# Kernel optimization log

Hardware: AMD Instinct MI355X
Metric: run time of the kernel (lower is better)

## Reference

```python
import jax, jax.numpy as jnp
import numpy as np

HIDDEN = 128
INPUT_DIM = 1
NUM_CLASSES = 2


def setup_inputs() -> dict:
    key = jax.random.key(0)
    ks = jax.random.split(key, 7)
    B, T = 256, 1024
    s_ih = 1.0 / np.sqrt(HIDDEN)
    x = jax.random.normal(ks[0], (B, T, INPUT_DIM), dtype=jnp.float32)
    W_ih = jax.random.uniform(ks[1], (HIDDEN, INPUT_DIM), jnp.float32, -s_ih, s_ih)
    W_hh = jax.random.uniform(ks[2], (HIDDEN, HIDDEN), jnp.float32, -s_ih, s_ih)
    b_ih = jax.random.uniform(ks[3], (HIDDEN,), jnp.float32, -s_ih, s_ih)
    b_hh = jax.random.uniform(ks[4], (HIDDEN,), jnp.float32, -s_ih, s_ih)
    W_fc = jax.random.uniform(ks[5], (NUM_CLASSES, HIDDEN), jnp.float32, -s_ih, s_ih)
    b_fc = jax.random.uniform(ks[6], (NUM_CLASSES,), jnp.float32, -s_ih, s_ih)
    return {"x": x, "W_ih": W_ih, "W_hh": W_hh, "b_ih": b_ih,
            "b_hh": b_hh, "W_fc": W_fc, "b_fc": b_fc}


def reference(x, W_ih, W_hh, b_ih, b_hh, W_fc, b_fc):
    B = x.shape[0]
    # Precompute input projection for all timesteps: [B,T,H]
    xp = jnp.einsum('bti,hi->bth', x, W_ih) + b_ih + b_hh
    h0 = jnp.zeros((B, HIDDEN), dtype=x.dtype)

    def step(h, xp_t):
        h_new = jnp.tanh(xp_t + h @ W_hh.T)  # [B,H]
        return h_new, h_new

    _, hs = jax.lax.scan(step, h0, jnp.swapaxes(xp, 0, 1))  # hs: [T,B,H]
    out = jnp.swapaxes(hs, 0, 1)  # [B,T,H]
    logits = jnp.einsum('bth,ch->btc', out, W_fc) + b_fc  # [B,T,C]
    return logits
```

## Files before the change

kernel.cpp:

```cpp
#include <hip/hip_runtime.h>

typedef float f32x2 __attribute__((ext_vector_type(2)));
typedef float f32x4 __attribute__((ext_vector_type(4)));

#define BB 256
#define TT 1024
#define HH 128
#define CC 2

__device__ __forceinline__ float ftanh(float u) {
    float e = __expf(2.0f * u);
    float r = __builtin_amdgcn_rcpf(e + 1.0f);
    return fmaf(-2.0f, r, 1.0f);
}

__device__ __forceinline__ float bcast(float v, int j) {
    return __int_as_float(__builtin_amdgcn_readlane(__float_as_int(v), j));
}

#define DPP_ADD(v, ctrl)                                                     \
    ((v) + __int_as_float(__builtin_amdgcn_mov_dpp(                          \
         __float_as_int(v), (ctrl), 0xF, 0xF, true)))

__global__ __launch_bounds__(256, 1) void rnn_kernel(
    const float* __restrict__ x, const float* __restrict__ W_ih,
    const float* __restrict__ W_hh, const float* __restrict__ b_ih,
    const float* __restrict__ b_hh, const float* __restrict__ W_fc,
    const float* __restrict__ b_fc, float* __restrict__ out)
{
    const int b   = blockIdx.x;
    const int tid = threadIdx.x;
    const int l   = tid & 63;
    const int wv  = tid >> 6;
    const int lq  = l & 31;
    const int kb  = wv << 5;
    const int rA  = l, rB = l + 64;
    const int rF  = kb + lq;

    __shared__ float xs[TT + 8];
    __shared__ f32x2 p2[2][4][64];
    __shared__ f32x2 qp[4][4];
    __shared__ f32x2 obuf[16];

    {
        const f32x4* xr = (const f32x4*)(x + (size_t)b * TT);
        ((f32x4*)xs)[tid] = xr[tid];
    }
    if (tid < 8) xs[TT + tid] = 0.f;

    const float wih  = W_ih[rF];
    const float bias = b_ih[rF] + b_hh[rF];
    const float wfs  = (l < 32) ? W_fc[rF] : W_fc[HH + rF];
    const float bf0  = b_fc[0], bf1 = b_fc[1];

    float wa[32], wb[32];
    {
        const f32x4* a4 = (const f32x4*)(W_hh + (size_t)rA * HH + kb);
        const f32x4* b4 = (const f32x4*)(W_hh + (size_t)rB * HH + kb);
        #pragma unroll
        for (int j = 0; j < 8; ++j) {
            f32x4 va = a4[j], vb = b4[j];
            wa[4*j+0] = va.x; wa[4*j+1] = va.y; wa[4*j+2] = va.z; wa[4*j+3] = va.w;
            wb[4*j+0] = vb.x; wb[4*j+1] = vb.y; wb[4*j+2] = vb.z; wb[4*j+3] = vb.w;
        }
        #pragma unroll
        for (int k = 0; k < 32; ++k)
            asm volatile("" : "+v"(wa[k]), "+v"(wb[k]));
    }

    float hn = 0.f;
    float* o = out + (size_t)b * TT * CC;

    __syncthreads();
    float xcur = xs[0];

    #pragma unroll 4
    for (int t = 0; t < TT; ++t) {
        const int buf = t & 1, qb = t & 3;

        float aA0 = 0.f, aA1 = 0.f, aB0 = 0.f, aB1 = 0.f;
        #pragma unroll
        for (int k = 0; k < 32; k += 2) {
            float s0 = bcast(hn, k);
            float s1 = bcast(hn, k + 1);
            aA0 = fmaf(wa[k],     s0, aA0);
            aB0 = fmaf(wb[k],     s0, aB0);
            aA1 = fmaf(wa[k + 1], s1, aA1);
            aB1 = fmaf(wb[k + 1], s1, aB1);
        }
        p2[buf][wv][l] = f32x2{ aA0 + aA1, aB0 + aB1 };
        const float xnext = xs[t + 1];

        __syncthreads();

        const float* pf = (const float*)&p2[buf][0][0]
                        + ((((wv & 1) << 5) + lq) << 1) + (wv >> 1);
        float p0 = pf[0], p1 = pf[128], pv2 = pf[256], pv3 = pf[384];

        {
            float q = wfs * hn;
            q = DPP_ADD(q, 0xB1);
            q = DPP_ADD(q, 0x4E);
            q = DPP_ADD(q, 0x124);
            q = DPP_ADD(q, 0x128);
            float q0 = bcast(q, 0)  + bcast(q, 16);
            float q1 = bcast(q, 32) + bcast(q, 48);
            if (l == 0) qp[qb][wv] = f32x2{q0, q1};
        }
        if (t >= 2 && tid == 0) {
            const int pq = (t - 1) & 3;
            f32x2 s = (qp[pq][0] + qp[pq][1]) + (qp[pq][2] + qp[pq][3]);
            s.x += bf0; s.y += bf1;
            obuf[(t - 2) & 15] = s;
        }
        if ((t & 15) == 1 && t >= 17 && tid < 32) {
            ((float*)(o + (t - 17) * CC))[tid] = ((const float*)obuf)[tid];
        }

        const float base = fmaf(xcur, wih, bias);
        xcur = xnext;
        hn = ftanh(base + ((p0 + p1) + (pv2 + pv3)));
    }

    {
        float q = wfs * hn;
        q = DPP_ADD(q, 0xB1);
        q = DPP_ADD(q, 0x4E);
        q = DPP_ADD(q, 0x124);
        q = DPP_ADD(q, 0x128);
        float q0 = bcast(q, 0)  + bcast(q, 16);
        float q1 = bcast(q, 32) + bcast(q, 48);
        if (l == 0) qp[0][wv] = f32x2{q0, q1};
    }
    __syncthreads();
    if (tid == 0) {
        f32x2 s = (qp[3][0] + qp[3][1]) + (qp[3][2] + qp[3][3]);
        s.x += bf0; s.y += bf1;
        *(f32x2*)(o + (TT - 2) * CC) = s;
        f32x2 s2 = (qp[0][0] + qp[0][1]) + (qp[0][2] + qp[0][3]);
        s2.x += bf0; s2.y += bf1;
        *(f32x2*)(o + (TT - 1) * CC) = s2;
    }
    if (tid < 28) {
        ((float*)(o + 1008 * CC))[tid] = ((const float*)obuf)[tid];
    }
}

extern "C" void kernel_launch(void* const* d_in, const int* in_sizes, int n_in,
                              void* d_out, int out_size, void* d_ws, size_t ws_size,
                              hipStream_t stream) {
    const float* x    = (const float*)d_in[0];
    const float* W_ih = (const float*)d_in[1];
    const float* W_hh = (const float*)d_in[2];
    const float* b_ih = (const float*)d_in[3];
    const float* b_hh = (const float*)d_in[4];
    const float* W_fc = (const float*)d_in[5];
    const float* b_fc = (const float*)d_in[6];
    float* out = (float*)d_out;

    rnn_kernel<<<BB, 256, 0, stream>>>(x, W_ih, W_hh, b_ih, b_hh, W_fc, b_fc, out);
}
```

Measured before the change: 441.7 us.

## Run each batch row's recurrence in one wavefront with LDS hidden-state ring

Each batch row now uses a single 64-lane wavefront that holds the full W_hh (two rows per lane, 256 VGPRs) instead of four wavefronts that split the K dimension. The new hidden state goes into a 16-deep LDS ring and is read back as float4 broadcasts, with packed f32x2 FMAs. This removes the per-step __syncthreads and the cross-wave partial-sum exchange. The output projection is batched every 16 steps across lanes. The risks are heavy register pressure, with possible spills, and LDS read latency on the serial critical path. Correctness also relies on a single wave giving implicit ordering of LDS accesses without barriers.

```diff
diff --git a/kernel.cpp b/kernel.cpp
--- a/kernel.cpp
+++ b/kernel.cpp
@@ -14,135 +14,100 @@
     return fmaf(-2.0f, r, 1.0f);
 }
 
-__device__ __forceinline__ float bcast(float v, int j) {
-    return __int_as_float(__builtin_amdgcn_readlane(__float_as_int(v), j));
+__device__ __forceinline__ f32x2 pkfma(f32x2 a, f32x2 b, f32x2 c) {
+    return (f32x2){fmaf(a.x, b.x, c.x), fmaf(a.y, b.y, c.y)};
 }
 
-#define DPP_ADD(v, ctrl)                                                     \
-    ((v) + __int_as_float(__builtin_amdgcn_mov_dpp(                          \
-         __float_as_int(v), (ctrl), 0xF, 0xF, true)))
-
-__global__ __launch_bounds__(256, 1) void rnn_kernel(
+__global__ __launch_bounds__(64, 1) void rnn_kernel(
     const float* __restrict__ x, const float* __restrict__ W_ih,
     const float* __restrict__ W_hh, const float* __restrict__ b_ih,
     const float* __restrict__ b_hh, const float* __restrict__ W_fc,
     const float* __restrict__ b_fc, float* __restrict__ out)
 {
-    const int b   = blockIdx.x;
-    const int tid = threadIdx.x;
-    const int l   = tid & 63;
-    const int wv  = tid >> 6;
-    const int lq  = l & 31;
-    const int kb  = wv << 5;
-    const int rA  = l, rB = l + 64;
-    const int rF  = kb + lq;
+    const int b = blockIdx.x;
+    const int l = threadIdx.x;
 
-    __shared__ float xs[TT + 8];
-    __shared__ f32x2 p2[2][4][64];
-    __shared__ f32x2 qp[4][4];
-    __shared__ f32x2 obuf[16];
+    __shared__ float xs[TT + 4];
+    __shared__ float hring[16][132];
 
     {
         const f32x4* xr = (const f32x4*)(x + (size_t)b * TT);
-        ((f32x4*)xs)[tid] = xr[tid];
+        f32x4* xd = (f32x4*)xs;
+        #pragma unroll
+        for (int i = 0; i < 4; ++i) xd[i * 64 + l] = xr[i * 64 + l];
     }
-    if (tid < 8) xs[TT + tid] = 0.f;
+    if (l < 4) xs[TT + l] = 0.f;
+    hring[15][l] = 0.f;
+    hring[15][l + 64] = 0.f;
 
-    const float wih  = W_ih[rF];
-    const float bias = b_ih[rF] + b_hh[rF];
-    const float wfs  = (l < 32) ? W_fc[rF] : W_fc[HH + rF];
-    const float bf0  = b_fc[0], bf1 = b_fc[1];
-
-    float wa[32], wb[32];
+    f32x2 wA[64], wB[64];
     {
-        const f32x4* a4 = (const f32x4*)(W_hh + (size_t)rA * HH + kb);
-        const f32x4* b4 = (const f32x4*)(W_hh + (size_t)rB * HH + kb);
+        const f32x2* a2 = (const f32x2*)(W_hh + (size_t)l * HH);
+        const f32x2* b2 = (const f32x2*)(W_hh + (size_t)(l + 64) * HH);
         #pragma unroll
-        for (int j = 0; j < 8; ++j) {
-            f32x4 va = a4[j], vb = b4[j];
-            wa[4*j+0] = va.x; wa[4*j+1] = va.y; wa[4*j+2] = va.z; wa[4*j+3] = va.w;
-            wb[4*j+0] = vb.x; wb[4*j+1] = vb.y; wb[4*j+2] = vb.z; wb[4*j+3] = vb.w;
-        }
+        for (int j = 0; j < 64; ++j) { wA[j] = a2[j]; wB[j] = b2[j]; }
         #pragma unroll
-        for (int k = 0; k < 32; ++k)
-            asm volatile("" : "+v"(wa[k]), "+v"(wb[k]));
+        for (int j = 0; j < 64; ++j)
+            asm volatile("" : "+v"(wA[j]), "+v"(wB[j]));
     }
 
-    float hn = 0.f;
+    const f32x2 wih2  = (f32x2){W_ih[l], W_ih[l + 64]};
+    const f32x2 bias2 = (f32x2){b_ih[l] + b_hh[l], b_ih[l + 64] + b_hh[l + 64]};
+
+    const int lc = l & 1;
+    const int lt = (l >> 1) & 15;
+    const int lh = l >> 5;
+    const f32x4* wf4 = (const f32x4*)(W_fc + lc * HH + lh * 64);
+    const float bfc = b_fc[lc];
     float* o = out + (size_t)b * TT * CC;
 
     __syncthreads();
+
     float xcur = xs[0];
 
-    #pragma unroll 4
     for (int t = 0; t < TT; ++t) {
-        const int buf = t & 1, qb = t & 3;
+        const f32x4* h4 = (const f32x4*)hring[(t + 15) & 15];
 
-        float aA0 = 0.f, aA1 = 0.f, aB0 = 0.f, aB1 = 0.f;
+        f32x2 aA0 = (f32x2){0.f, 0.f}, aA1 = aA0, aB0 = aA0, aB1 = aA0;
         #pragma unroll
-        for (int k = 0; k < 32; k += 2) {
-            float s0 = bcast(hn, k);
-            float s1 = bcast(hn, k + 1);
-            aA0 = fmaf(wa[k],     s0, aA0);
-            aB0 = fmaf(wb[k],     s0, aB0);
-            aA1 = fmaf(wa[k + 1], s1, aA1);
-            aB1 = fmaf(wb[k + 1], s1, aB1);
-        }
-        p2[buf][wv][l] = f32x2{ aA0 + aA1, aB0 + aB1 };
-        const float xnext = xs[t + 1];
-
-        __syncthreads();
-
-        const float* pf = (const float*)&p2[buf][0][0]
-                        + ((((wv & 1) << 5) + lq) << 1) + (wv >> 1);
-        float p0 = pf[0], p1 = pf[128], pv2 = pf[256], pv3 = pf[384];
-
-        {
-            float q = wfs * hn;
-            q = DPP_ADD(q, 0xB1);
-            q = DPP_ADD(q, 0x4E);
-            q = DPP_ADD(q, 0x124);
-            q = DPP_ADD(q, 0x128);
-            float q0 = bcast(q, 0)  + bcast(q, 16);
-            float q1 = bcast(q, 32) + bcast(q, 48);
-            if (l == 0) qp[qb][wv] = f32x2{q0, q1};
-        }
-        if (t >= 2 && tid == 0) {
-            const int pq = (t - 1) & 3;
-            f32x2 s = (qp[pq][0] + qp[pq][1]) + (qp[pq][2] + qp[pq][3]);
-            s.x += bf0; s.y += bf1;
-            obuf[(t - 2) & 15] = s;
-        }
-        if ((t & 15) == 1 && t >= 17 && tid < 32) {
-            ((float*)(o + (t - 17) * CC))[tid] = ((const float*)obuf)[tid];
+        for (int j = 0; j < 32; ++j) {
+            const f32x4 hv = h4[j];
+            const f32x2 hlo = (f32x2){hv.x, hv.y};
+            const f32x2 hhi = (f32x2){hv.z, hv.w};
+            aA0 = pkfma(wA[2 * j],     hlo, aA0);
+            aA1 = pkfma(wA[2 * j + 1], hhi, aA1);
+            aB0 = pkfma(wB[2 * j],     hlo, aB0);
+            aB1 = pkfma(wB[2 * j + 1], hhi, aB1);
         }
 
-        const float base = fmaf(xcur, wih, bias);
+        const float xnext = xs[t + 1];
+        const f32x2 base = pkfma((f32x2){xcur, xcur}, wih2, bias2);
         xcur = xnext;
-        hn = ftanh(base + ((p0 + p1) + (pv2 + pv3)));
-    }
 
-    {
-        float q = wfs * hn;
-        q = DPP_ADD(q, 0xB1);
-        q = DPP_ADD(q, 0x4E);
-        q = DPP_ADD(q, 0x124);
-        q = DPP_ADD(q, 0x128);
-        float q0 = bcast(q, 0)  + bcast(q, 16);
-        float q1 = bcast(q, 32) + bcast(q, 48);
-        if (l == 0) qp[0][wv] = f32x2{q0, q1};
-    }
-    __syncthreads();
-    if (tid == 0) {
-        f32x2 s = (qp[3][0] + qp[3][1]) + (qp[3][2] + qp[3][3]);
-        s.x += bf0; s.y += bf1;
-        *(f32x2*)(o + (TT - 2) * CC) = s;
-        f32x2 s2 = (qp[0][0] + qp[0][1]) + (qp[0][2] + qp[0][3]);
-        s2.x += bf0; s2.y += bf1;
-        *(f32x2*)(o + (TT - 1) * CC) = s2;
-    }
-    if (tid < 28) {
-        ((float*)(o + 1008 * CC))[tid] = ((const float*)obuf)[tid];
+        const float sA = (aA0.x + aA0.y) + (aA1.x + aA1.y);
+        const float sB = (aB0.x + aB0.y) + (aB1.x + aB1.y);
+        const float hA = ftanh(base.x + sA);
+        const float hB = ftanh(base.y + sB);
+
+        float* hw = hring[t & 15];
+        hw[l] = hA;
+        hw[l + 64] = hB;
+
+        if ((t & 15) == 15) {
+            const f32x4* hb = (const f32x4*)(&hring[lt][lh * 64]);
+            f32x2 q0 = (f32x2){0.f, 0.f}, q1 = q0;
+            #pragma unroll
+            for (int j = 0; j < 16; ++j) {
+                const f32x4 hv = hb[j];
+                const f32x4 wv = wf4[j];
+                q0 = pkfma((f32x2){wv.x, wv.y}, (f32x2){hv.x, hv.y}, q0);
+                q1 = pkfma((f32x2){wv.z, wv.w}, (f32x2){hv.z, hv.w}, q1);
+            }
+            const f32x2 qs = q0 + q1;
+            float q = qs.x + qs.y;
+            q += __shfl_xor(q, 32);
+            if (l < 32) o[(t - 15) * CC + l] = q + bfc;
+        }
     }
 }
 
@@ -158,5 +123,5 @@
     const float* b_fc = (const float*)d_in[6];
     float* out = (float*)d_out;
 
-    rnn_kernel<<<BB, 256, 0, stream>>>(x, W_ih, W_hh, b_ih, b_hh, W_fc, b_fc, out);
+    rnn_kernel<<<BB, 64, 0, stream>>>(x, W_ih, W_hh, b_ih, b_hh, W_fc, b_fc, out);
 }
```

Measured after the change: 1.539 ms. 3.48x slower.
